# Kernel tuning notes

Hardware: AMD Instinct MI355X
Metric: run time of the kernel (lower is better)

## Reference

```python
import jax, jax.numpy as jnp
import numpy as np

B, S, H = 1, 1024, 2880
NQ, NKV, D = 64, 8, 64          # query heads, kv heads, head_dim
G = NQ // NKV                    # GQA group size
W = 128                          # sliding window
SCALE = D ** -0.5
NEG = -1e30


def rotate_half(x):
    x1, x2 = jnp.split(x, 2, axis=-1)
    return jnp.concatenate((-x2, x1), axis=-1)


def setup_inputs() -> dict:
    key = jax.random.key(0)
    ks = jax.random.split(key, 8)
    hidden_states = jax.random.normal(ks[0], (B, S, H), jnp.float32)
    # rotary tables, half head_dim (module concats (cos,cos) to full dim)
    pos = jnp.arange(S, dtype=jnp.float32)[:, None]
    inv = 1.0 / (10000.0 ** (jnp.arange(0, D, 2, dtype=jnp.float32) / D))
    ang = pos * inv[None, :]                      # (S, D/2)
    cos = jnp.cos(ang)[None].astype(jnp.float32)  # (1, S, D/2)
    sin = jnp.sin(ang)[None].astype(jnp.float32)
    w_qkv = jax.random.normal(ks[1], (H, (NQ + 2 * NKV) * D), jnp.float32) * 0.02
    b_qkv = jax.random.normal(ks[2], ((NQ + 2 * NKV) * D,), jnp.float32) * 0.02
    w_o = jax.random.normal(ks[3], (NQ * D, H), jnp.float32) * 0.02
    b_o = jax.random.normal(ks[4], (H,), jnp.float32) * 0.02
    sinks = jax.random.normal(ks[5], (NQ,), jnp.float32)
    k_cache = jnp.zeros((B, S, NKV, D), jnp.float32)
    v_cache = jnp.zeros((B, S, NKV, D), jnp.float32)
    return {"hidden_states": hidden_states, "cos": cos, "sin": sin,
            "w_qkv": w_qkv, "b_qkv": b_qkv, "w_o": w_o, "b_o": b_o,
            "sinks": sinks, "k_cache": k_cache, "v_cache": v_cache, "kv_len": 0}


def reference(hidden_states, cos, sin, w_qkv, b_qkv, w_o, b_o, sinks,
              k_cache, v_cache, kv_len):
    # fused QKV projection + split
    qkv = hidden_states @ w_qkv + b_qkv                      # (B, S, (NQ+2*NKV)*D)
    q, k, v = jnp.split(qkv, [NQ * D, NQ * D + NKV * D], axis=-1)
    q = q.reshape(B, S, NQ, D)
    k = k.reshape(B, S, NKV, D)
    v = v.reshape(B, S, NKV, D)
    # RoPE (BSND layout, half-dim tables duplicated to full dim)
    cosf = jnp.concatenate((cos, cos), axis=-1)[:, :, None, :]
    sinf = jnp.concatenate((sin, sin), axis=-1)[:, :, None, :]
    q = q * cosf + rotate_half(q) * sinf
    k = k * cosf + rotate_half(k) * sinf
    # KV-cache scatter update at position kv_len along seq dim
    k_cache = jax.lax.dynamic_update_slice(k_cache, k, (0, kv_len, 0, 0))
    v_cache = jax.lax.dynamic_update_slice(v_cache, v, (0, kv_len, 0, 0))
    T = kv_len + S
    keys = k_cache[:, :T]                                    # (B, T, NKV, D)
    vals = v_cache[:, :T]
    # GQA: group query heads by kv head
    qg = q.reshape(B, S, NKV, G, D)
    scores = jnp.einsum('bqhgd,bkhd->bhgqk', qg, keys) * SCALE  # (B,NKV,G,S,T)
    # causal + sliding-window mask
    i = jnp.arange(S)[:, None] + kv_len
    j = jnp.arange(T)[None, :]
    allowed = (j <= i) & (i - j < W)
    scores = jnp.where(allowed, scores, NEG)
    # softmax with per-head learnable sink logit (sink gets no value)
    sk = sinks.reshape(NKV, G)[None, :, :, None]             # (1,NKV,G,1)
    m = jnp.maximum(jnp.max(scores, axis=-1), sk)            # (B,NKV,G,S)
    p = jnp.exp(scores - m[..., None])
    denom = jnp.sum(p, axis=-1) + jnp.exp(sk - m)
    attn = jnp.einsum('bhgqk,bkhd->bqhgd', p / denom[..., None], vals)
    out = attn.reshape(B, S, NQ * D) @ w_o + b_o             # (B, S, H)
    return out
```

## Files before the change

### kernel.cpp

```cpp
#include <hip/hip_runtime.h>
#include <hip/hip_bf16.h>

#define NQH 64
#define NKVH 8
#define DH 64
#define SEQ 1024
#define HID 2880
#define QKV_N 5120
#define ATTN_N 4096
#define WIN 128
#define WO_NPAD 3072
#define SCALE_F 0.125f

typedef __attribute__((ext_vector_type(8))) __bf16 bf16x8;
typedef __attribute__((ext_vector_type(4))) float f32x4;

#define GLOAD_LDS16(g, l) \
    __builtin_amdgcn_global_load_lds((const __attribute__((address_space(1))) void*)(g), \
                                     (__attribute__((address_space(3))) void*)(l), 16, 0, 0)

__device__ __forceinline__ ushort f2bf(float x) {
    union { float f; unsigned int u; } c; c.f = x;
    unsigned int u = c.u;
    unsigned int r = (u + 0x7FFFu + ((u >> 16) & 1u)) >> 16;
    return (ushort)r;
}

__global__ __launch_bounds__(256) void convert_f32_bf16(
    const float* __restrict__ in, ushort* __restrict__ out, int n4)
{
    int idx = blockIdx.x * blockDim.x + threadIdx.x;
    int stride = gridDim.x * blockDim.x;
    for (int i = idx; i < n4; i += stride) {
        float4 v = reinterpret_cast<const float4*>(in)[i];
        ushort4 o;
        o.x = f2bf(v.x); o.y = f2bf(v.y); o.z = f2bf(v.z); o.w = f2bf(v.w);
        reinterpret_cast<ushort4*>(out)[i] = o;
    }
}

__global__ __launch_bounds__(256) void transpose_convert(
    const float* __restrict__ in, ushort* __restrict__ out, int K, int N)
{
    __shared__ ushort tile[64][80];
    const int bk = blockIdx.x * 64;
    const int bn = blockIdx.y * 64;
    const int tid = threadIdx.x;
    const bool inb = bn < N;

#pragma unroll
    for (int it = 0; it < 4; ++it) {
        int r = it * 16 + (tid >> 4);
        int c4 = (tid & 15) * 4;
        float4 v = make_float4(0.f, 0.f, 0.f, 0.f);
        if (inb) v = *(const float4*)&in[(size_t)(bk + r) * N + bn + c4];
        tile[c4 + 0][r] = f2bf(v.x);
        tile[c4 + 1][r] = f2bf(v.y);
        tile[c4 + 2][r] = f2bf(v.z);
        tile[c4 + 3][r] = f2bf(v.w);
    }
    __syncthreads();
#pragma unroll
    for (int it = 0; it < 2; ++it) {
        int nr = it * 32 + (tid >> 3);
        int c8 = (tid & 7) * 8;
        uint4 v = *(const uint4*)&tile[nr][c8];
        *(uint4*)&out[(size_t)(bn + nr) * K + bk + c8] = v;
    }
}

template<int BM, int BN, int WAVES_N>
__global__ __launch_bounds__(512) void gemm_bal(
    const ushort* __restrict__ A, const ushort* __restrict__ BT,
    const float* __restrict__ bias, float* __restrict__ C,
    int K, int ldC, int Nreal)
{
    constexpr int WAVES_M = 8 / WAVES_N;
    constexpr int WM = BM / WAVES_M;
    constexpr int WN = BN / WAVES_N;
    constexpr int MR = WM / 16;
    constexpr int NR = WN / 16;
    constexpr int ASZ = BM * 64;
    constexpr int BSZ = BN * 64;
    constexpr int ACH = BM * 8;
    constexpr int TOTCH = (BM + BN) * 8;
    constexpr int NLOAD = (TOTCH + 511) / 512;

    __shared__ ushort Al[2 * ASZ];
    __shared__ ushort Bl[2 * BSZ];

    const int t = threadIdx.x;
    const int lane = t & 63;
    const int w = t >> 6;
    const int wr = w / WAVES_N;
    const int wc = w % WAVES_N;
    const int g4 = lane >> 4;
    const int r15 = lane & 15;

    const int nx = gridDim.x;
    const int flat = blockIdx.x + nx * blockIdx.y;
    const int per = (nx * gridDim.y) >> 3;
    const int virt = (flat & 7) * per + (flat >> 3);
    const int n0 = (virt % nx) * BN;
    const int m0 = (virt / nx) * BM;

    const ushort* src[NLOAD];
    ushort* d0[NLOAD];
    ushort* d1[NLOAD];
#pragma unroll
    for (int i = 0; i < NLOAD; ++i) {
        int lin = i * 512 + t;
        src[i] = nullptr; d0[i] = nullptr; d1[i] = nullptr;
        if (lin < ACH) {
            int row = lin >> 3, ch = (lin & 7) ^ (row & 7);
            src[i] = A + (size_t)(m0 + row) * K + ch * 8;
            d0[i] = &Al[lin * 8];
            d1[i] = &Al[ASZ + lin * 8];
        } else if (lin < TOTCH) {
            int l2 = lin - ACH;
            int row = l2 >> 3, ch = (l2 & 7) ^ (row & 7);
            src[i] = BT + (size_t)(n0 + row) * K + ch * 8;
            d0[i] = &Bl[l2 * 8];
            d1[i] = &Bl[BSZ + l2 * 8];
        }
    }

#define STAGE_TILE(buf) do { \
        _Pragma("unroll") \
        for (int i = 0; i < NLOAD; ++i) \
            if (src[i]) { \
                GLOAD_LDS16(src[i], (buf) ? d1[i] : d0[i]); \
                src[i] += 64; \
            } \
    } while (0)

    int aoff[MR][2], boff[NR][2];
#pragma unroll
    for (int mi = 0; mi < MR; ++mi)
#pragma unroll
        for (int ks = 0; ks < 2; ++ks) {
            int row = wr * WM + mi * 16 + r15;
            aoff[mi][ks] = row * 64 + (((ks * 4 + g4) ^ (row & 7)) * 8);
        }
#pragma unroll
    for (int ni = 0; ni < NR; ++ni)
#pragma unroll
        for (int ks = 0; ks < 2; ++ks) {
            int col = wc * WN + ni * 16 + r15;
            boff[ni][ks] = col * 64 + (((ks * 4 + g4) ^ (col & 7)) * 8);
        }

    f32x4 acc[MR][NR];
#pragma unroll
    for (int mi = 0; mi < MR; ++mi)
#pragma unroll
        for (int ni = 0; ni < NR; ++ni) acc[mi][ni] = (f32x4){0.f, 0.f, 0.f, 0.f};

#define COMPUTE_TILE(buf) do { \
        const ushort* Ab = &Al[(buf) * ASZ]; \
        const ushort* Bb = &Bl[(buf) * BSZ]; \
        _Pragma("unroll") \
        for (int ks = 0; ks < 2; ++ks) { \
            bf16x8 af[MR], bfr[NR]; \
            _Pragma("unroll") \
            for (int mi = 0; mi < MR; ++mi) af[mi] = *(const bf16x8*)&Ab[aoff[mi][ks]]; \
            _Pragma("unroll") \
            for (int ni = 0; ni < NR; ++ni) bfr[ni] = *(const bf16x8*)&Bb[boff[ni][ks]]; \
            _Pragma("unroll") \
            for (int mi = 0; mi < MR; ++mi) \
                _Pragma("unroll") \
                for (int ni = 0; ni < NR; ++ni) \
                    acc[mi][ni] = __builtin_amdgcn_mfma_f32_16x16x32_bf16(af[mi], bfr[ni], acc[mi][ni], 0, 0, 0); \
        } \
    } while (0)

    const int NT = K >> 6;
    STAGE_TILE(0);
    __syncthreads();
    for (int kt = 0; kt < NT; kt += 2) {
        if (kt + 1 < NT) STAGE_TILE(1);
        COMPUTE_TILE(0);
        __syncthreads();
        if (kt + 1 < NT) {
            if (kt + 2 < NT) STAGE_TILE(0);
            COMPUTE_TILE(1);
            __syncthreads();
        }
    }
#undef STAGE_TILE
#undef COMPUTE_TILE

#pragma unroll
    for (int ni = 0; ni < NR; ++ni) {
        int col = n0 + wc * WN + ni * 16 + r15;
        if (col < Nreal) {
            float bv = bias[col];
#pragma unroll
            for (int mi = 0; mi < MR; ++mi) {
                int row = m0 + wr * WM + mi * 16 + g4 * 4;
#pragma unroll
                for (int r = 0; r < 4; ++r)
                    C[(size_t)(row + r) * ldC + col] = acc[mi][ni][r] + bv;
            }
        }
    }
}

__global__ __launch_bounds__(512) void attn_mfma_kernel(
    const float* __restrict__ qkv, const float* __restrict__ sinks,
    const float* __restrict__ cosp, const float* __restrict__ sinp,
    ushort* __restrict__ attn_out)
{
    __shared__ __align__(16) ushort Kl[160][72];
    __shared__ __align__(16) ushort Vt[64][168];
    __shared__ __align__(16) ushort Pl[8][32][40];
    const int t = threadIdx.x;
    const int w = t >> 6;
    const int l = t & 63;
    const int g4 = l >> 4;
    const int r15 = l & 15;
    const int q0 = blockIdx.x * 32;
    const int hk = blockIdx.y;
    const int kbase = q0 - 128;

#pragma unroll
    for (int i = 0; i < 5; ++i) {
        int idx = i * 512 + t;
        int row = idx >> 4;
        int c4 = (idx & 15) * 4;
        int j = kbase + row;
        float4 kr = make_float4(0.f, 0.f, 0.f, 0.f);
        float4 vv = make_float4(0.f, 0.f, 0.f, 0.f);
        if (j >= 0) {
            const float* kb = &qkv[(size_t)j * QKV_N + 4096 + hk * 64];
            float4 kx = *(const float4*)&kb[c4];
            float4 ky = *(const float4*)&kb[c4 ^ 32];
            float4 cs = *(const float4*)&cosp[j * 32 + (c4 & 31)];
            float4 sn = *(const float4*)&sinp[j * 32 + (c4 & 31)];
            if (c4 < 32) {
                kr.x = kx.x * cs.x - ky.x * sn.x; kr.y = kx.y * cs.y - ky.y * sn.y;
                kr.z = kx.z * cs.z - ky.z * sn.z; kr.w = kx.w * cs.w - ky.w * sn.w;
            } else {
                kr.x = kx.x * cs.x + ky.x * sn.x; kr.y = kx.y * cs.y + ky.y * sn.y;
                kr.z = kx.z * cs.z + ky.z * sn.z; kr.w = kx.w * cs.w + ky.w * sn.w;
            }
            vv = *(const float4*)&qkv[(size_t)j * QKV_N + 4608 + hk * 64 + c4];
        }
        ushort4 kp;
        kp.x = f2bf(kr.x); kp.y = f2bf(kr.y); kp.z = f2bf(kr.z); kp.w = f2bf(kr.w);
        *(ushort4*)&Kl[row][c4] = kp;
        Vt[c4 + 0][row] = f2bf(vv.x);
        Vt[c4 + 1][row] = f2bf(vv.y);
        Vt[c4 + 2][row] = f2bf(vv.z);
        Vt[c4 + 3][row] = f2bf(vv.w);
    }

    bf16x8 qf[2][2];
#pragma unroll
    for (int ct = 0; ct < 2; ++ct) {
        int R = w * 32 + ct * 16 + r15;
        int q = q0 + (R & 31);
        int hq = hk * 8 + (R >> 5);
        const float* qb = &qkv[(size_t)q * QKV_N + hq * 64];
        int d8 = g4 * 8;
        float4 a0 = *(const float4*)&qb[d8];
        float4 b0 = *(const float4*)&qb[d8 + 4];
        float4 a1 = *(const float4*)&qb[32 + d8];
        float4 b1 = *(const float4*)&qb[32 + d8 + 4];
        float4 c0 = *(const float4*)&cosp[q * 32 + d8];
        float4 c1 = *(const float4*)&cosp[q * 32 + d8 + 4];
        float4 s0 = *(const float4*)&sinp[q * 32 + d8];
        float4 s1 = *(const float4*)&sinp[q * 32 + d8 + 4];
        union { ushort u[8]; bf16x8 v; } p0, p1;
        p0.u[0] = f2bf((a0.x * c0.x - a1.x * s0.x) * SCALE_F);
        p0.u[1] = f2bf((a0.y * c0.y - a1.y * s0.y) * SCALE_F);
        p0.u[2] = f2bf((a0.z * c0.z - a1.z * s0.z) * SCALE_F);
        p0.u[3] = f2bf((a0.w * c0.w - a1.w * s0.w) * SCALE_F);
        p0.u[4] = f2bf((b0.x * c1.x - b1.x * s1.x) * SCALE_F);
        p0.u[5] = f2bf((b0.y * c1.y - b1.y * s1.y) * SCALE_F);
        p0.u[6] = f2bf((b0.z * c1.z - b1.z * s1.z) * SCALE_F);
        p0.u[7] = f2bf((b0.w * c1.w - b1.w * s1.w) * SCALE_F);
        p1.u[0] = f2bf((a1.x * c0.x + a0.x * s0.x) * SCALE_F);
        p1.u[1] = f2bf((a1.y * c0.y + a0.y * s0.y) * SCALE_F);
        p1.u[2] = f2bf((a1.z * c0.z + a0.z * s0.z) * SCALE_F);
        p1.u[3] = f2bf((a1.w * c0.w + a0.w * s0.w) * SCALE_F);
        p1.u[4] = f2bf((b1.x * c1.x + b0.x * s1.x) * SCALE_F);
        p1.u[5] = f2bf((b1.y * c1.y + b0.y * s1.y) * SCALE_F);
        p1.u[6] = f2bf((b1.z * c1.z + b0.z * s1.z) * SCALE_F);
        p1.u[7] = f2bf((b1.w * c1.w + b0.w * s1.w) * SCALE_F);
        qf[ct][0] = p0.v;
        qf[ct][1] = p1.v;
    }
    __syncthreads();

    f32x4 sc[10][2];
#pragma unroll
    for (int kt = 0; kt < 10; ++kt) {
        sc[kt][0] = (f32x4){0.f, 0.f, 0.f, 0.f};
        sc[kt][1] = (f32x4){0.f, 0.f, 0.f, 0.f};
    }
#pragma unroll
    for (int kt = 0; kt < 10; ++kt) {
#pragma unroll
        for (int s = 0; s < 2; ++s) {
            bf16x8 kf = *(const bf16x8*)&Kl[kt * 16 + r15][s * 32 + g4 * 8];
            sc[kt][0] = __builtin_amdgcn_mfma_f32_16x16x32_bf16(kf, qf[0][s], sc[kt][0], 0, 0, 0);
            sc[kt][1] = __builtin_amdgcn_mfma_f32_16x16x32_bf16(kf, qf[1][s], sc[kt][1], 0, 0, 0);
        }
    }

    const int minkey = 128 - q0;
#pragma unroll
    for (int ct = 0; ct < 2; ++ct) {
        int R = w * 32 + ct * 16 + r15;
        int ql = R & 31;
        float snk = sinks[hk * 8 + (R >> 5)];
#pragma unroll
        for (int kt = 0; kt < 10; ++kt)
#pragma unroll
            for (int r = 0; r < 4; ++r) {
                int key = kt * 16 + g4 * 4 + r;
                bool ok = (key > ql) && (key <= ql + 128) && (key >= minkey);
                if (!ok) sc[kt][ct][r] = -1e30f;
            }
        float m = snk;
#pragma unroll
        for (int kt = 0; kt < 10; ++kt)
#pragma unroll
            for (int r = 0; r < 4; ++r) m = fmaxf(m, sc[kt][ct][r]);
        m = fmaxf(m, __shfl_xor(m, 16));
        m = fmaxf(m, __shfl_xor(m, 32));
        float sum = 0.f;
#pragma unroll
        for (int kt = 0; kt < 10; ++kt)
#pragma unroll
            for (int r = 0; r < 4; ++r) {
                float p = __expf(sc[kt][ct][r] - m);
                sc[kt][ct][r] = p;
                sum += p;
            }
        sum += __shfl_xor(sum, 16);
        sum += __shfl_xor(sum, 32);
        sum += __expf(snk - m);
        float iv = 1.0f / sum;
#pragma unroll
        for (int kt = 0; kt < 10; ++kt)
#pragma unroll
            for (int r = 0; r < 4; ++r) sc[kt][ct][r] *= iv;
    }

    f32x4 pv[2][4];
#pragma unroll
    for (int mi = 0; mi < 2; ++mi)
#pragma unroll
        for (int ni = 0; ni < 4; ++ni) pv[mi][ni] = (f32x4){0.f, 0.f, 0.f, 0.f};

#pragma unroll
    for (int s = 0; s < 5; ++s) {
#pragma unroll
        for (int ct = 0; ct < 2; ++ct)
#pragma unroll
            for (int kh = 0; kh < 2; ++kh) {
                int kt = 2 * s + kh;
                ushort4 p4;
                p4.x = f2bf(sc[kt][ct][0]);
                p4.y = f2bf(sc[kt][ct][1]);
                p4.z = f2bf(sc[kt][ct][2]);
                p4.w = f2bf(sc[kt][ct][3]);
                *(ushort4*)&Pl[w][ct * 16 + r15][kh * 16 + g4 * 4] = p4;
            }
#pragma unroll
        for (int mi = 0; mi < 2; ++mi) {
            bf16x8 pf = *(const bf16x8*)&Pl[w][mi * 16 + r15][g4 * 8];
#pragma unroll
            for (int ni = 0; ni < 4; ++ni) {
                bf16x8 vf = *(const bf16x8*)&Vt[ni * 16 + r15][s * 32 + g4 * 8];
                pv[mi][ni] = __builtin_amdgcn_mfma_f32_16x16x32_bf16(pf, vf, pv[mi][ni], 0, 0, 0);
            }
        }
    }

#pragma unroll
    for (int mi = 0; mi < 2; ++mi)
#pragma unroll
        for (int r = 0; r < 4; ++r) {
            int R = w * 32 + mi * 16 + g4 * 4 + r;
            int q = q0 + (R & 31);
            int hq = hk * 8 + (R >> 5);
            ushort* ob = &attn_out[(size_t)q * ATTN_N + hq * 64 + r15];
#pragma unroll
            for (int ni = 0; ni < 4; ++ni)
                ob[ni * 16] = f2bf(pv[mi][ni][r]);
        }
}

extern "C" void kernel_launch(void* const* d_in, const int* in_sizes, int n_in,
                              void* d_out, int out_size, void* d_ws, size_t ws_size,
                              hipStream_t stream)
{
    const float* hidden = (const float*)d_in[0];
    const float* cosp   = (const float*)d_in[1];
    const float* sinp   = (const float*)d_in[2];
    const float* w_qkv  = (const float*)d_in[3];
    const float* b_qkv  = (const float*)d_in[4];
    const float* w_o    = (const float*)d_in[5];
    const float* b_o    = (const float*)d_in[6];
    const float* sinks  = (const float*)d_in[7];

    char* ws = (char*)d_ws;
    size_t off = 0;
    ushort* wqkvT = (ushort*)(ws + off); off += (size_t)QKV_N * HID * 2;
    ushort* woT   = (ushort*)(ws + off); off += (size_t)WO_NPAD * ATTN_N * 2;
    float*  qkv   = (float*)(ws + off);  off += (size_t)SEQ * QKV_N * 4;
    ushort* hidden_b = (ushort*)(ws + off);
    ushort* attn_b   = (ushort*)(ws + off); off += (size_t)SEQ * ATTN_N * 2;
    if (off > ws_size) return;

    transpose_convert<<<dim3(HID / 64, QKV_N / 64), 256, 0, stream>>>(w_qkv, wqkvT, HID, QKV_N);
    transpose_convert<<<dim3(ATTN_N / 64, WO_NPAD / 64), 256, 0, stream>>>(w_o, woT, ATTN_N, HID);
    convert_f32_bf16<<<2048, 256, 0, stream>>>(hidden, hidden_b, SEQ * HID / 4);

    gemm_bal<128, 80, 1><<<dim3(QKV_N / 80, SEQ / 128), 512, 0, stream>>>(
        hidden_b, wqkvT, b_qkv, qkv, HID, QKV_N, QKV_N);

    attn_mfma_kernel<<<dim3(SEQ / 32, NKVH), 512, 0, stream>>>(
        qkv, sinks, cosp, sinp, attn_b);

    gemm_bal<64, 96, 2><<<dim3(WO_NPAD / 96, SEQ / 64), 512, 0, stream>>>(
        attn_b, woT, b_o, (float*)d_out, ATTN_N, HID, HID);
}
```

Measured before the change: 140.8 us.

## Fuse weight transpose and bf16 conversion into GEMM B-tile loading

```diff
diff --git a/kernel.cpp b/kernel.cpp
--- a/kernel.cpp
+++ b/kernel.cpp
@@ -9,7 +9,6 @@
 #define QKV_N 5120
 #define ATTN_N 4096
 #define WIN 128
-#define WO_NPAD 3072
 #define SCALE_F 0.125f
 
 typedef __attribute__((ext_vector_type(8))) __bf16 bf16x8;
@@ -39,39 +38,9 @@
     }
 }
 
-__global__ __launch_bounds__(256) void transpose_convert(
-    const float* __restrict__ in, ushort* __restrict__ out, int K, int N)
-{
-    __shared__ ushort tile[64][80];
-    const int bk = blockIdx.x * 64;
-    const int bn = blockIdx.y * 64;
-    const int tid = threadIdx.x;
-    const bool inb = bn < N;
-
-#pragma unroll
-    for (int it = 0; it < 4; ++it) {
-        int r = it * 16 + (tid >> 4);
-        int c4 = (tid & 15) * 4;
-        float4 v = make_float4(0.f, 0.f, 0.f, 0.f);
-        if (inb) v = *(const float4*)&in[(size_t)(bk + r) * N + bn + c4];
-        tile[c4 + 0][r] = f2bf(v.x);
-        tile[c4 + 1][r] = f2bf(v.y);
-        tile[c4 + 2][r] = f2bf(v.z);
-        tile[c4 + 3][r] = f2bf(v.w);
-    }
-    __syncthreads();
-#pragma unroll
-    for (int it = 0; it < 2; ++it) {
-        int nr = it * 32 + (tid >> 3);
-        int c8 = (tid & 7) * 8;
-        uint4 v = *(const uint4*)&tile[nr][c8];
-        *(uint4*)&out[(size_t)(bn + nr) * K + bk + c8] = v;
-    }
-}
-
 template<int BM, int BN, int WAVES_N>
-__global__ __launch_bounds__(512) void gemm_bal(
-    const ushort* __restrict__ A, const ushort* __restrict__ BT,
+__global__ __launch_bounds__(512) void gemm_ft(
+    const ushort* __restrict__ A, const float* __restrict__ Bsrc, int Nsrc,
     const float* __restrict__ bias, float* __restrict__ C,
     int K, int ldC, int Nreal)
 {
@@ -83,8 +52,9 @@
     constexpr int ASZ = BM * 64;
     constexpr int BSZ = BN * 64;
     constexpr int ACH = BM * 8;
-    constexpr int TOTCH = (BM + BN) * 8;
-    constexpr int NLOAD = (TOTCH + 511) / 512;
+    constexpr int NLOADA = (ACH + 511) / 512;
+    constexpr int BSLOT = (BN / 4) * 32;
+    constexpr int NLOADB = (BSLOT + 511) / 512;
 
     __shared__ ushort Al[2 * ASZ];
     __shared__ ushort Bl[2 * BSZ];
@@ -103,34 +73,82 @@
     const int virt = (flat & 7) * per + (flat >> 3);
     const int n0 = (virt % nx) * BN;
     const int m0 = (virt / nx) * BM;
-
-    const ushort* src[NLOAD];
-    ushort* d0[NLOAD];
-    ushort* d1[NLOAD];
-#pragma unroll
-    for (int i = 0; i < NLOAD; ++i) {
+    const bool binb = (n0 < Nreal);
+
+    const ushort* aSrc[NLOADA];
+    ushort* aD0[NLOADA];
+    ushort* aD1[NLOADA];
+#pragma unroll
+    for (int i = 0; i < NLOADA; ++i) {
         int lin = i * 512 + t;
-        src[i] = nullptr; d0[i] = nullptr; d1[i] = nullptr;
+        aSrc[i] = nullptr; aD0[i] = nullptr; aD1[i] = nullptr;
         if (lin < ACH) {
             int row = lin >> 3, ch = (lin & 7) ^ (row & 7);
-            src[i] = A + (size_t)(m0 + row) * K + ch * 8;
-            d0[i] = &Al[lin * 8];
-            d1[i] = &Al[ASZ + lin * 8];
-        } else if (lin < TOTCH) {
-            int l2 = lin - ACH;
-            int row = l2 >> 3, ch = (l2 & 7) ^ (row & 7);
-            src[i] = BT + (size_t)(n0 + row) * K + ch * 8;
-            d0[i] = &Bl[l2 * 8];
-            d1[i] = &Bl[BSZ + l2 * 8];
-        }
-    }
-
-#define STAGE_TILE(buf) do { \
+            aSrc[i] = A + (size_t)(m0 + row) * K + ch * 8;
+            aD0[i] = &Al[lin * 8];
+            aD1[i] = &Al[ASZ + lin * 8];
+        }
+    }
+
+    const float* bSrc[NLOADB];
+    int wOff[NLOADB][4];
+    float4 bf0[NLOADB], bf1[NLOADB];
+#pragma unroll
+    for (int i = 0; i < NLOADB; ++i) {
+        int s = i * 512 + t;
+        bSrc[i] = nullptr;
+        if (s < BSLOT) {
+            int k2 = s / (BN / 4);
+            int n4 = (s % (BN / 4)) * 4;
+            int k = 2 * k2;
+            bSrc[i] = Bsrc + (size_t)k * Nsrc + n0 + n4;
+#pragma unroll
+            for (int j = 0; j < 4; ++j) {
+                int n = n4 + j;
+                int sg = (n + (n >> 3)) & 7;
+                wOff[i][j] = n * 64 + (((k >> 3) ^ sg) * 8) + (k & 7);
+            }
+        }
+    }
+
+#define B_LOAD() do { \
         _Pragma("unroll") \
-        for (int i = 0; i < NLOAD; ++i) \
-            if (src[i]) { \
-                GLOAD_LDS16(src[i], (buf) ? d1[i] : d0[i]); \
-                src[i] += 64; \
+        for (int i = 0; i < NLOADB; ++i) \
+            if (bSrc[i]) { \
+                if (binb) { \
+                    bf0[i] = *(const float4*)bSrc[i]; \
+                    bf1[i] = *(const float4*)(bSrc[i] + Nsrc); \
+                } else { \
+                    bf0[i] = make_float4(0.f, 0.f, 0.f, 0.f); \
+                    bf1[i] = make_float4(0.f, 0.f, 0.f, 0.f); \
+                } \
+                bSrc[i] += (size_t)64 * Nsrc; \
+            } \
+    } while (0)
+
+#define B_WRITE(buf) do { \
+        ushort* Bb_ = &Bl[(buf) * BSZ]; \
+        _Pragma("unroll") \
+        for (int i = 0; i < NLOADB; ++i) \
+            if (bSrc[i]) { \
+                unsigned int v_; \
+                v_ = (unsigned int)f2bf(bf0[i].x) | ((unsigned int)f2bf(bf1[i].x) << 16); \
+                *(unsigned int*)&Bb_[wOff[i][0]] = v_; \
+                v_ = (unsigned int)f2bf(bf0[i].y) | ((unsigned int)f2bf(bf1[i].y) << 16); \
+                *(unsigned int*)&Bb_[wOff[i][1]] = v_; \
+                v_ = (unsigned int)f2bf(bf0[i].z) | ((unsigned int)f2bf(bf1[i].z) << 16); \
+                *(unsigned int*)&Bb_[wOff[i][2]] = v_; \
+                v_ = (unsigned int)f2bf(bf0[i].w) | ((unsigned int)f2bf(bf1[i].w) << 16); \
+                *(unsigned int*)&Bb_[wOff[i][3]] = v_; \
+            } \
+    } while (0)
+
+#define A_STAGE(buf) do { \
+        _Pragma("unroll") \
+        for (int i = 0; i < NLOADA; ++i) \
+            if (aSrc[i]) { \
+                GLOAD_LDS16(aSrc[i], (buf) ? aD1[i] : aD0[i]); \
+                aSrc[i] += 64; \
             } \
     } while (0)
 
@@ -147,7 +165,8 @@
 #pragma unroll
         for (int ks = 0; ks < 2; ++ks) {
             int col = wc * WN + ni * 16 + r15;
-            boff[ni][ks] = col * 64 + (((ks * 4 + g4) ^ (col & 7)) * 8);
+            int sg = (col + (col >> 3)) & 7;
+            boff[ni][ks] = col * 64 + (((ks * 4 + g4) ^ sg) * 8);
         }
 
     f32x4 acc[MR][NR];
@@ -175,19 +194,25 @@
     } while (0)
 
     const int NT = K >> 6;
-    STAGE_TILE(0);
+    B_LOAD();
+    A_STAGE(0);
+    B_WRITE(0);
     __syncthreads();
     for (int kt = 0; kt < NT; kt += 2) {
-        if (kt + 1 < NT) STAGE_TILE(1);
+        if (kt + 1 < NT) { B_LOAD(); A_STAGE(1); }
         COMPUTE_TILE(0);
+        if (kt + 1 < NT) B_WRITE(1);
         __syncthreads();
         if (kt + 1 < NT) {
-            if (kt + 2 < NT) STAGE_TILE(0);
+            if (kt + 2 < NT) { B_LOAD(); A_STAGE(0); }
             COMPUTE_TILE(1);
+            if (kt + 2 < NT) B_WRITE(0);
             __syncthreads();
         }
     }
-#undef STAGE_TILE
+#undef B_LOAD
+#undef B_WRITE
+#undef A_STAGE
 #undef COMPUTE_TILE
 
 #pragma unroll
@@ -409,23 +434,19 @@
 
     char* ws = (char*)d_ws;
     size_t off = 0;
-    ushort* wqkvT = (ushort*)(ws + off); off += (size_t)QKV_N * HID * 2;
-    ushort* woT   = (ushort*)(ws + off); off += (size_t)WO_NPAD * ATTN_N * 2;
     float*  qkv   = (float*)(ws + off);  off += (size_t)SEQ * QKV_N * 4;
     ushort* hidden_b = (ushort*)(ws + off);
     ushort* attn_b   = (ushort*)(ws + off); off += (size_t)SEQ * ATTN_N * 2;
     if (off > ws_size) return;
 
-    transpose_convert<<<dim3(HID / 64, QKV_N / 64), 256, 0, stream>>>(w_qkv, wqkvT, HID, QKV_N);
-    transpose_convert<<<dim3(ATTN_N / 64, WO_NPAD / 64), 256, 0, stream>>>(w_o, woT, ATTN_N, HID);
     convert_f32_bf16<<<2048, 256, 0, stream>>>(hidden, hidden_b, SEQ * HID / 4);
 
-    gemm_bal<128, 80, 1><<<dim3(QKV_N / 80, SEQ / 128), 512, 0, stream>>>(
-        hidden_b, wqkvT, b_qkv, qkv, HID, QKV_N, QKV_N);
+    gemm_ft<128, 80, 1><<<dim3(QKV_N / 80, SEQ / 128), 512, 0, stream>>>(
+        hidden_b, w_qkv, QKV_N, b_qkv, qkv, HID, QKV_N, QKV_N);
 
     attn_mfma_kernel<<<dim3(SEQ / 32, NKVH), 512, 0, stream>>>(
         qkv, sinks, cosp, sinp, attn_b);
 
-    gemm_bal<64, 96, 2><<<dim3(WO_NPAD / 96, SEQ / 64), 512, 0, stream>>>(
-        attn_b, woT, b_o, (float*)d_out, ATTN_N, HID, HID);
+    gemm_ft<64, 96, 2><<<dim3(3072 / 96, SEQ / 64), 512, 0, stream>>>(
+        attn_b, w_o, HID, b_o, (float*)d_out, ATTN_N, HID, HID);
 }
```

After: 163.1 us. +15.9%, slower.

## Load GEMM A operand directly into registers instead of staging through LDS

Applied to the files above, without the earlier changes.

```diff
diff --git a/kernel.cpp b/kernel.cpp
--- a/kernel.cpp
+++ b/kernel.cpp
@@ -70,7 +70,7 @@
 }
 
 template<int BM, int BN, int WAVES_N>
-__global__ __launch_bounds__(512) void gemm_bal(
+__global__ __launch_bounds__(512) void gemm_ra(
     const ushort* __restrict__ A, const ushort* __restrict__ BT,
     const float* __restrict__ bias, float* __restrict__ C,
     int K, int ldC, int Nreal)
@@ -80,13 +80,10 @@
     constexpr int WN = BN / WAVES_N;
     constexpr int MR = WM / 16;
     constexpr int NR = WN / 16;
-    constexpr int ASZ = BM * 64;
     constexpr int BSZ = BN * 64;
-    constexpr int ACH = BM * 8;
-    constexpr int TOTCH = (BM + BN) * 8;
-    constexpr int NLOAD = (TOTCH + 511) / 512;
-
-    __shared__ ushort Al[2 * ASZ];
+    constexpr int BCH = BN * 8;
+    constexpr int NLOADB = (BCH + 511) / 512;
+
     __shared__ ushort Bl[2 * BSZ];
 
     const int t = threadIdx.x;
@@ -104,44 +101,50 @@
     const int n0 = (virt % nx) * BN;
     const int m0 = (virt / nx) * BM;
 
-    const ushort* src[NLOAD];
-    ushort* d0[NLOAD];
-    ushort* d1[NLOAD];
-#pragma unroll
-    for (int i = 0; i < NLOAD; ++i) {
+    const ushort* bSrc[NLOADB];
+    ushort* bD0[NLOADB];
+    ushort* bD1[NLOADB];
+#pragma unroll
+    for (int i = 0; i < NLOADB; ++i) {
         int lin = i * 512 + t;
-        src[i] = nullptr; d0[i] = nullptr; d1[i] = nullptr;
-        if (lin < ACH) {
+        bSrc[i] = nullptr; bD0[i] = nullptr; bD1[i] = nullptr;
+        if (lin < BCH) {
             int row = lin >> 3, ch = (lin & 7) ^ (row & 7);
-            src[i] = A + (size_t)(m0 + row) * K + ch * 8;
-            d0[i] = &Al[lin * 8];
-            d1[i] = &Al[ASZ + lin * 8];
-        } else if (lin < TOTCH) {
-            int l2 = lin - ACH;
-            int row = l2 >> 3, ch = (l2 & 7) ^ (row & 7);
-            src[i] = BT + (size_t)(n0 + row) * K + ch * 8;
-            d0[i] = &Bl[l2 * 8];
-            d1[i] = &Bl[BSZ + l2 * 8];
-        }
-    }
-
-#define STAGE_TILE(buf) do { \
+            bSrc[i] = BT + (size_t)(n0 + row) * K + ch * 8;
+            bD0[i] = &Bl[lin * 8];
+            bD1[i] = &Bl[BSZ + lin * 8];
+        }
+    }
+
+#define B_STAGE(buf) do { \
         _Pragma("unroll") \
-        for (int i = 0; i < NLOAD; ++i) \
-            if (src[i]) { \
-                GLOAD_LDS16(src[i], (buf) ? d1[i] : d0[i]); \
-                src[i] += 64; \
+        for (int i = 0; i < NLOADB; ++i) \
+            if (bSrc[i]) { \
+                GLOAD_LDS16(bSrc[i], (buf) ? bD1[i] : bD0[i]); \
+                bSrc[i] += 64; \
             } \
     } while (0)
 
-    int aoff[MR][2], boff[NR][2];
+    const ushort* aP[MR][2];
 #pragma unroll
     for (int mi = 0; mi < MR; ++mi)
 #pragma unroll
-        for (int ks = 0; ks < 2; ++ks) {
-            int row = wr * WM + mi * 16 + r15;
-            aoff[mi][ks] = row * 64 + (((ks * 4 + g4) ^ (row & 7)) * 8);
-        }
+        for (int ks = 0; ks < 2; ++ks)
+            aP[mi][ks] = A + (size_t)(m0 + wr * WM + mi * 16 + r15) * K + (ks * 4 + g4) * 8;
+
+    bf16x8 ar[2][MR][2];
+
+#define A_LOAD(buf) do { \
+        _Pragma("unroll") \
+        for (int mi = 0; mi < MR; ++mi) \
+            _Pragma("unroll") \
+            for (int ks = 0; ks < 2; ++ks) { \
+                ar[buf][mi][ks] = *(const bf16x8*)aP[mi][ks]; \
+                aP[mi][ks] += 64; \
+            } \
+    } while (0)
+
+    int boff[NR][2];
 #pragma unroll
     for (int ni = 0; ni < NR; ++ni)
 #pragma unroll
@@ -157,37 +160,36 @@
         for (int ni = 0; ni < NR; ++ni) acc[mi][ni] = (f32x4){0.f, 0.f, 0.f, 0.f};
 
 #define COMPUTE_TILE(buf) do { \
-        const ushort* Ab = &Al[(buf) * ASZ]; \
         const ushort* Bb = &Bl[(buf) * BSZ]; \
         _Pragma("unroll") \
         for (int ks = 0; ks < 2; ++ks) { \
-            bf16x8 af[MR], bfr[NR]; \
-            _Pragma("unroll") \
-            for (int mi = 0; mi < MR; ++mi) af[mi] = *(const bf16x8*)&Ab[aoff[mi][ks]]; \
+            bf16x8 bfr[NR]; \
             _Pragma("unroll") \
             for (int ni = 0; ni < NR; ++ni) bfr[ni] = *(const bf16x8*)&Bb[boff[ni][ks]]; \
             _Pragma("unroll") \
             for (int mi = 0; mi < MR; ++mi) \
                 _Pragma("unroll") \
                 for (int ni = 0; ni < NR; ++ni) \
-                    acc[mi][ni] = __builtin_amdgcn_mfma_f32_16x16x32_bf16(af[mi], bfr[ni], acc[mi][ni], 0, 0, 0); \
+                    acc[mi][ni] = __builtin_amdgcn_mfma_f32_16x16x32_bf16(ar[buf][mi][ks], bfr[ni], acc[mi][ni], 0, 0, 0); \
         } \
     } while (0)
 
     const int NT = K >> 6;
-    STAGE_TILE(0);
+    B_STAGE(0);
+    A_LOAD(0);
     __syncthreads();
     for (int kt = 0; kt < NT; kt += 2) {
-        if (kt + 1 < NT) STAGE_TILE(1);
+        if (kt + 1 < NT) { B_STAGE(1); A_LOAD(1); }
         COMPUTE_TILE(0);
         __syncthreads();
         if (kt + 1 < NT) {
-            if (kt + 2 < NT) STAGE_TILE(0);
+            if (kt + 2 < NT) { B_STAGE(0); A_LOAD(0); }
             COMPUTE_TILE(1);
             __syncthreads();
         }
     }
-#undef STAGE_TILE
+#undef B_STAGE
+#undef A_LOAD
 #undef COMPUTE_TILE
 
 #pragma unroll
@@ -420,12 +422,12 @@
     transpose_convert<<<dim3(ATTN_N / 64, WO_NPAD / 64), 256, 0, stream>>>(w_o, woT, ATTN_N, HID);
     convert_f32_bf16<<<2048, 256, 0, stream>>>(hidden, hidden_b, SEQ * HID / 4);
 
-    gemm_bal<128, 80, 1><<<dim3(QKV_N / 80, SEQ / 128), 512, 0, stream>>>(
+    gemm_ra<128, 80, 1><<<dim3(QKV_N / 80, SEQ / 128), 512, 0, stream>>>(
         hidden_b, wqkvT, b_qkv, qkv, HID, QKV_N, QKV_N);
 
     attn_mfma_kernel<<<dim3(SEQ / 32, NKVH), 512, 0, stream>>>(
         qkv, sinks, cosp, sinp, attn_b);
 
-    gemm_bal<64, 96, 2><<<dim3(WO_NPAD / 96, SEQ / 64), 512, 0, stream>>>(
+    gemm_ra<64, 96, 2><<<dim3(WO_NPAD / 96, SEQ / 64), 512, 0, stream>>>(
         attn_b, woT, b_o, (float*)d_out, ATTN_N, HID, HID);
 }
```

Result: slower. 177.5 us (+26.1%).
